# Kernel tuning notes

Hardware: AMD Instinct MI355X
Metric: run time of the kernel (lower is better)

Reference implementation:

```python
import jax, jax.numpy as jnp
import numpy as np

N_NODES = 100000
N_EDGES = 1600000
IN_DIM, FEAT_DIM, HID_DIM, OUT_DIM = 128, 64, 64, 32


def _lin_params(key, fan_in, fan_out, bias=True):
    k1, k2 = jax.random.split(key)
    bound = 1.0 / np.sqrt(fan_in)
    W = jax.random.uniform(k1, (fan_out, fan_in), jnp.float32, -bound, bound)
    if bias:
        b = jax.random.uniform(k2, (fan_out,), jnp.float32, -bound, bound)
        return W, b
    return W


def setup_inputs() -> dict:
    key = jax.random.key(0)
    ks = jax.random.split(key, 10)
    x = jax.random.normal(ks[0], (N_NODES, IN_DIM), jnp.float32)
    edge_index = jax.random.randint(ks[1], (2, N_EDGES), 0, N_NODES, jnp.int64 if jax.config.jax_enable_x64 else jnp.int32)
    W_pre, b_pre = _lin_params(ks[2], IN_DIM, FEAT_DIM)
    Wl1, bl1 = _lin_params(ks[3], FEAT_DIM, HID_DIM)
    Wr1 = _lin_params(ks[4], FEAT_DIM, HID_DIM, bias=False)
    Wl2, bl2 = _lin_params(ks[5], HID_DIM, HID_DIM)
    Wr2 = _lin_params(ks[6], HID_DIM, HID_DIM, bias=False)
    Wl3, bl3 = _lin_params(ks[7], HID_DIM, OUT_DIM)
    Wr3 = _lin_params(ks[8], HID_DIM, OUT_DIM, bias=False)
    return {"x": x, "edge_index": edge_index,
            "W_pre": W_pre, "b_pre": b_pre,
            "Wl1": Wl1, "bl1": bl1, "Wr1": Wr1,
            "Wl2": Wl2, "bl2": bl2, "Wr2": Wr2,
            "Wl3": Wl3, "bl3": bl3, "Wr3": Wr3}


def _sage_conv(x, src, dst, inv_deg, Wl, bl, Wr):
    # mean-aggregate neighbor features per destination node
    summed = jax.ops.segment_sum(x[src], dst, num_segments=N_NODES)  # [N, d]
    agg = summed * inv_deg                                           # [N, d]
    return agg @ Wl.T + bl + x @ Wr.T


def reference(x, edge_index, W_pre, b_pre, Wl1, bl1, Wr1, Wl2, bl2, Wr2, Wl3, bl3, Wr3):
    src, dst = edge_index[0], edge_index[1]
    deg = jax.ops.segment_sum(jnp.ones((N_EDGES,), x.dtype), dst, num_segments=N_NODES)
    inv_deg = (1.0 / jnp.maximum(deg, 1.0))[:, None]  # [N,1]

    h = x @ W_pre.T + b_pre                              # feature_pre
    h = jax.nn.relu(_sage_conv(h, src, dst, inv_deg, Wl1, bl1, Wr1))
    h = jax.nn.relu(_sage_conv(h, src, dst, inv_deg, Wl2, bl2, Wr2))
    h = _sage_conv(h, src, dst, inv_deg, Wl3, bl3, Wr3)
    # F.normalize(p=2, dim=-1)
    norm = jnp.maximum(jnp.linalg.norm(h, axis=-1, keepdims=True), 1e-12)
    return h / norm
```

## Files before the change

### kernel.cpp

```cpp
#include <hip/hip_runtime.h>

#define NN 100000
#define NE 1600000
#define NB 196
#define NPBK 512

static inline size_t alignup(size_t x) { return (x + 255) & ~(size_t)255; }

typedef __attribute__((ext_vector_type(8))) short bfrag;
typedef __attribute__((ext_vector_type(4))) float f32x4v;

__device__ __forceinline__ float bf_lo(unsigned u) { return __uint_as_float(u << 16); }
__device__ __forceinline__ float bf_hi(unsigned u) { return __uint_as_float(u & 0xFFFF0000u); }
__device__ __forceinline__ unsigned short f2bf(float f) {
    unsigned u = __float_as_uint(f);
    return (unsigned short)((u + 0x7FFFu + ((u >> 16) & 1u)) >> 16);
}
__device__ __forceinline__ unsigned pack2(float a, float b) {
    return (unsigned)f2bf(a) | ((unsigned)f2bf(b) << 16);
}

__global__ __launch_bounds__(256) void k_bcount(const int* __restrict__ dst,
                                                int* __restrict__ bcnt) {
    __shared__ int h[NB];
    int tid = threadIdx.x;
    for (int i = tid; i < NB; i += 256) h[i] = 0;
    __syncthreads();
    int i = blockIdx.x * 256 + tid;
    int stride = gridDim.x * 256;
    for (; i < NE; i += stride) atomicAdd(&h[dst[i] >> 9], 1);
    __syncthreads();
    for (int i2 = tid; i2 < NB; i2 += 256) {
        int c = h[i2];
        if (c) atomicAdd(&bcnt[i2], c);
    }
}

__global__ __launch_bounds__(256) void k_bscan(const int* __restrict__ bcnt,
                                               int* __restrict__ bbase,
                                               int* __restrict__ bcur,
                                               int* __restrict__ row_ptr) {
    __shared__ int tmp[256];
    int tid = threadIdx.x;
    int v = (tid < NB) ? bcnt[tid] : 0;
    tmp[tid] = v;
    __syncthreads();
    for (int off = 1; off < 256; off <<= 1) {
        int t = (tid >= off) ? tmp[tid - off] : 0;
        __syncthreads();
        tmp[tid] += t;
        __syncthreads();
    }
    int excl = tmp[tid] - v;
    if (tid < NB) { bbase[tid] = excl; bcur[tid] = excl; }
    if (tid == 0) row_ptr[NN] = NE;
}

#define EPT 16
__global__ __launch_bounds__(256) void k_bscatter(const int* __restrict__ src,
                                                  const int* __restrict__ dst,
                                                  int* __restrict__ bcur,
                                                  unsigned* __restrict__ ebuf) {
    __shared__ int h[NB], base[NB], pos[NB];
    int tid = threadIdx.x;
    for (int i = tid; i < NB; i += 256) h[i] = 0;
    __syncthreads();
    long e0 = (long)blockIdx.x * (256 * EPT);
    unsigned packed[EPT];
    int bk[EPT];
    #pragma unroll
    for (int j = 0; j < EPT; ++j) {
        long e = e0 + (long)j * 256 + tid;
        if (e < NE) {
            int s = src[e], d = dst[e];
            bk[j] = d >> 9;
            packed[j] = ((unsigned)(d & 511) << 17) | (unsigned)s;
            atomicAdd(&h[bk[j]], 1);
        } else bk[j] = -1;
    }
    __syncthreads();
    for (int i = tid; i < NB; i += 256) {
        int c = h[i];
        base[i] = c ? atomicAdd(&bcur[i], c) : 0;
        pos[i] = 0;
    }
    __syncthreads();
    #pragma unroll
    for (int j = 0; j < EPT; ++j) {
        if (bk[j] >= 0) {
            int p = atomicAdd(&pos[bk[j]], 1);
            ebuf[base[bk[j]] + p] = packed[j];
        }
    }
}

__global__ __launch_bounds__(256) void k_bcsr(const unsigned* __restrict__ ebuf,
                                              const int* __restrict__ bbase,
                                              int* __restrict__ row_ptr,
                                              float* __restrict__ inv_deg,
                                              int* __restrict__ col) {
    __shared__ int h[NPBK];
    __shared__ int psum[256];
    int b = blockIdx.x;
    int tid = threadIdx.x;
    int begin = bbase[b];
    int end = (b + 1 < NB) ? bbase[b + 1] : NE;
    for (int i = tid; i < NPBK; i += 256) h[i] = 0;
    __syncthreads();
    for (int e = begin + tid; e < end; e += 256) atomicAdd(&h[ebuf[e] >> 17], 1);
    __syncthreads();
    int a0 = h[2 * tid], a1 = h[2 * tid + 1];
    psum[tid] = a0 + a1;
    __syncthreads();
    for (int off = 1; off < 256; off <<= 1) {
        int t = (tid >= off) ? psum[tid - off] : 0;
        __syncthreads();
        psum[tid] += t;
        __syncthreads();
    }
    int pexcl = psum[tid] - (a0 + a1);
    int eo0 = pexcl, eo1 = pexcl + a0;
    int n0 = b * NPBK + 2 * tid, n1 = n0 + 1;
    if (n0 < NN) { row_ptr[n0] = begin + eo0; inv_deg[n0] = 1.0f / (float)((a0 > 1) ? a0 : 1); }
    if (n1 < NN) { row_ptr[n1] = begin + eo1; inv_deg[n1] = 1.0f / (float)((a1 > 1) ? a1 : 1); }
    __syncthreads();
    h[2 * tid] = eo0;
    h[2 * tid + 1] = eo1;
    __syncthreads();
    for (int e = begin + tid; e < end; e += 256) {
        unsigned p = ebuf[e];
        int dl = p >> 17;
        int s = (int)(p & 0x1FFFFu);
        int q = atomicAdd(&h[dl], 1);
        col[begin + q] = s;
    }
}

template <int K1, int K2, int M, bool RELU, bool NORM, bool ABF, bool OBF>
__global__ __launch_bounds__(256, 2) void k_mfma(const void* __restrict__ A1v,
                                                 const void* __restrict__ A2v,
                                                 const float* __restrict__ W1,
                                                 const float* __restrict__ W2,
                                                 const float* __restrict__ bias,
                                                 void* __restrict__ outv) {
    constexpr int K = K1 + K2;
    static_assert(K == 128, "K must be 128");
    constexpr int NT = M / 16;
    constexpr int SA = 136;
    constexpr int SW = 136;

    __shared__ __align__(16) unsigned short Ahi[64 * SA];
    __shared__ __align__(16) unsigned short Alo[ABF ? 1 : 64 * SA];
    __shared__ __align__(16) unsigned short Whi[M * SW];
    __shared__ __align__(16) unsigned short Wlo[M * SW];

    int tid = threadIdx.x;
    long nbase = (long)blockIdx.x * 64;

    for (int idx = tid; idx < M * 128; idx += 256) {
        int m = idx >> 7, k = idx & 127;
        float w = (K2 == 0 || k < K1) ? W1[m * K1 + k] : W2[m * K2 + (k - K1)];
        unsigned short hb = f2bf(w);
        float hf = __uint_as_float((unsigned)hb << 16);
        Whi[m * SW + k] = hb;
        Wlo[m * SW + k] = f2bf(w - hf);
    }
    if (ABF) {
        const unsigned short* A1 = (const unsigned short*)A1v;
        const unsigned short* A2 = (const unsigned short*)A2v;
        for (int idx = tid; idx < 64 * 16; idx += 256) {
            int row = idx >> 4, c8 = idx & 15;
            long n = nbase + row;
            uint4 v = make_uint4(0u, 0u, 0u, 0u);
            if (n < NN) v = (c8 < 8) ? ((const uint4*)(A1 + n * 64))[c8]
                                     : ((const uint4*)(A2 + n * 64))[c8 - 8];
            *(uint4*)&Ahi[row * SA + c8 * 8] = v;
        }
    } else {
        const float* A1 = (const float*)A1v;
        for (int idx = tid; idx < 64 * 32; idx += 256) {
            int row = idx >> 5, c4 = idx & 31;
            long n = nbase + row;
            float4 v = make_float4(0.f, 0.f, 0.f, 0.f);
            if (n < NN) v = ((const float4*)(A1 + n * 128))[c4];
            ushort4 h, l;
            h.x = f2bf(v.x); l.x = f2bf(v.x - __uint_as_float((unsigned)h.x << 16));
            h.y = f2bf(v.y); l.y = f2bf(v.y - __uint_as_float((unsigned)h.y << 16));
            h.z = f2bf(v.z); l.z = f2bf(v.z - __uint_as_float((unsigned)h.z << 16));
            h.w = f2bf(v.w); l.w = f2bf(v.w - __uint_as_float((unsigned)h.w << 16));
            *(ushort4*)&Ahi[row * SA + c4 * 4] = h;
            *(ushort4*)&Alo[row * SA + c4 * 4] = l;
        }
    }
    __syncthreads();

    const int l = tid & 63, wv = tid >> 6;
    const int row0 = wv * 16;
    const int mrow = l & 15, g = l >> 4;
    const int koff = g * 8;

    bfrag a[4], al[4];
    #pragma unroll
    for (int kk = 0; kk < 4; ++kk)
        a[kk] = *(const bfrag*)&Ahi[(row0 + mrow) * SA + kk * 32 + koff];
    if (!ABF) {
        #pragma unroll
        for (int kk = 0; kk < 4; ++kk)
            al[kk] = *(const bfrag*)&Alo[(row0 + mrow) * SA + kk * 32 + koff];
    }

    f32x4v acc[NT];
    #pragma unroll
    for (int c = 0; c < NT; ++c) {
        float bv = bias[c * 16 + mrow];
        acc[c][0] = bv; acc[c][1] = bv; acc[c][2] = bv; acc[c][3] = bv;
    }

    #pragma unroll
    for (int c = 0; c < NT; ++c) {
        #pragma unroll
        for (int kk = 0; kk < 4; ++kk) {
            bfrag bh = *(const bfrag*)&Whi[(c * 16 + mrow) * SW + kk * 32 + koff];
            bfrag bl = *(const bfrag*)&Wlo[(c * 16 + mrow) * SW + kk * 32 + koff];
            acc[c] = __builtin_amdgcn_mfma_f32_16x16x32_bf16(a[kk], bh, acc[c], 0, 0, 0);
            acc[c] = __builtin_amdgcn_mfma_f32_16x16x32_bf16(a[kk], bl, acc[c], 0, 0, 0);
            if (!ABF)
                acc[c] = __builtin_amdgcn_mfma_f32_16x16x32_bf16(al[kk], bh, acc[c], 0, 0, 0);
        }
    }

    if (RELU) {
        #pragma unroll
        for (int c = 0; c < NT; ++c)
            #pragma unroll
            for (int j = 0; j < 4; ++j) acc[c][j] = fmaxf(acc[c][j], 0.0f);
    }

    if (NORM) {
        #pragma unroll
        for (int j = 0; j < 4; ++j) {
            float s = 0.f;
            #pragma unroll
            for (int c = 0; c < NT; ++c) s += acc[c][j] * acc[c][j];
            s += __shfl_xor(s, 1);
            s += __shfl_xor(s, 2);
            s += __shfl_xor(s, 4);
            s += __shfl_xor(s, 8);
            float sc = 1.0f / fmaxf(sqrtf(s), 1e-12f);
            long n = nbase + row0 + g * 4 + j;
            if (n < NN) {
                float* outf = (float*)outv;
                #pragma unroll
                for (int c = 0; c < NT; ++c)
                    outf[n * M + c * 16 + mrow] = acc[c][j] * sc;
            }
        }
    } else {
        #pragma unroll
        for (int j = 0; j < 4; ++j) {
            long n = nbase + row0 + g * 4 + j;
            if (n >= NN) continue;
            #pragma unroll
            for (int c = 0; c < NT; ++c) {
                if (OBF) ((unsigned short*)outv)[n * M + c * 16 + mrow] = f2bf(acc[c][j]);
                else     ((float*)outv)[n * M + c * 16 + mrow] = acc[c][j];
            }
        }
    }
}

__global__ __launch_bounds__(256) void k_agg16(const unsigned* __restrict__ H,
                                               const int* __restrict__ row_ptr,
                                               const int* __restrict__ col,
                                               const float* __restrict__ inv_deg,
                                               unsigned* __restrict__ AGG) {
    int gt = blockIdx.x * 256 + threadIdx.x;
    int n = gt >> 5;
    int l = gt & 31;
    if (n >= NN) return;
    int beg = row_ptr[n], end = row_ptr[n + 1];
    float a0 = 0.f, a1 = 0.f;
    int e = beg;
    for (; e + 3 < end; e += 4) {
        int s0 = col[e], s1 = col[e + 1], s2 = col[e + 2], s3 = col[e + 3];
        unsigned u0 = H[(long)s0 * 32 + l];
        unsigned u1 = H[(long)s1 * 32 + l];
        unsigned u2 = H[(long)s2 * 32 + l];
        unsigned u3 = H[(long)s3 * 32 + l];
        a0 += bf_lo(u0) + bf_lo(u1) + bf_lo(u2) + bf_lo(u3);
        a1 += bf_hi(u0) + bf_hi(u1) + bf_hi(u2) + bf_hi(u3);
    }
    for (; e < end; ++e) {
        unsigned u = H[(long)col[e] * 32 + l];
        a0 += bf_lo(u);
        a1 += bf_hi(u);
    }
    float w = inv_deg[n];
    AGG[(long)n * 32 + l] = pack2(a0 * w, a1 * w);
}

extern "C" void kernel_launch(void* const* d_in, const int* in_sizes, int n_in,
                              void* d_out, int out_size, void* d_ws, size_t ws_size,
                              hipStream_t stream) {
    const float* x      = (const float*)d_in[0];
    const int*   edges  = (const int*)d_in[1];
    const float* W_pre  = (const float*)d_in[2];
    const float* b_pre  = (const float*)d_in[3];
    const float* Wl1    = (const float*)d_in[4];
    const float* bl1    = (const float*)d_in[5];
    const float* Wr1    = (const float*)d_in[6];
    const float* Wl2    = (const float*)d_in[7];
    const float* bl2    = (const float*)d_in[8];
    const float* Wr2    = (const float*)d_in[9];
    const float* Wl3    = (const float*)d_in[10];
    const float* bl3    = (const float*)d_in[11];
    const float* Wr3    = (const float*)d_in[12];
    float* out = (float*)d_out;

    const int* src = edges;
    const int* dst = edges + NE;

    char* w = (char*)d_ws;
    int*      row_ptr = (int*)w;      w += alignup((NN + 1) * 4);
    float*    inv_deg = (float*)w;    w += alignup(NN * 4);
    int*      bcnt    = (int*)w;      w += alignup(NB * 4);
    int*      bbase   = (int*)w;      w += alignup(NB * 4);
    int*      bcur    = (int*)w;      w += alignup(NB * 4);
    unsigned* ebuf    = (unsigned*)w; w += alignup((size_t)NE * 4);
    int*      col     = (int*)w;      w += alignup((size_t)NE * 4);
    unsigned short* bufA = (unsigned short*)w; w += alignup((size_t)NN * 64 * 2);
    unsigned short* bufB = (unsigned short*)w; w += alignup((size_t)NN * 64 * 2);
    unsigned short* bufC = (unsigned short*)w; w += alignup((size_t)NN * 64 * 2);

    hipMemsetAsync(bcnt, 0, NB * sizeof(int), stream);
    k_bcount<<<1024, 256, 0, stream>>>(dst, bcnt);
    k_bscan<<<1, 256, 0, stream>>>(bcnt, bbase, bcur, row_ptr);
    k_bscatter<<<(NE + 4095) / 4096, 256, 0, stream>>>(src, dst, bcur, ebuf);
    k_bcsr<<<NB, 256, 0, stream>>>(ebuf, bbase, row_ptr, inv_deg, col);

    const int GRID = (NN + 63) / 64;

    k_mfma<128, 0, 64, false, false, false, true>
        <<<GRID, 256, 0, stream>>>(x, nullptr, W_pre, nullptr, b_pre, bufA);

    k_agg16<<<(NN * 32 + 255) / 256, 256, 0, stream>>>((unsigned*)bufA, row_ptr, col, inv_deg, (unsigned*)bufB);
    k_mfma<64, 64, 64, true, false, true, true>
        <<<GRID, 256, 0, stream>>>(bufB, bufA, Wl1, Wr1, bl1, bufC);

    k_agg16<<<(NN * 32 + 255) / 256, 256, 0, stream>>>((unsigned*)bufC, row_ptr, col, inv_deg, (unsigned*)bufB);
    k_mfma<64, 64, 64, true, false, true, true>
        <<<GRID, 256, 0, stream>>>(bufB, bufC, Wl2, Wr2, bl2, bufA);

    k_agg16<<<(NN * 32 + 255) / 256, 256, 0, stream>>>((unsigned*)bufA, row_ptr, col, inv_deg, (unsigned*)bufB);
    k_mfma<64, 64, 32, false, true, true, false>
        <<<GRID, 256, 0, stream>>>(bufB, bufA, Wl3, Wr3, bl3, out);
}
```

Measured before the change: 384.4 us.

## Fuse neighbor mean aggregation into SAGE MFMA kernels

Removes the separate aggregation kernel and the intermediate AGG buffer. Each SAGE-layer block now gathers neighbor rows for its 64 nodes straight into shared memory before the MFMA GEMM, and the gather loop is unrolled by 8. This saves a global write and read of the aggregate plus three launches. In exchange, gather latency now sits inside a GEMM kernel with heavy shared-memory use, so fewer gather threads are in flight (occupancy hint raised to 3 blocks), and degree imbalance within a block can stall the MFMA phase.

```diff
diff --git a/kernel.cpp b/kernel.cpp
--- a/kernel.cpp
+++ b/kernel.cpp
@@ -136,21 +136,13 @@
     }
 }
 
-template <int K1, int K2, int M, bool RELU, bool NORM, bool ABF, bool OBF>
-__global__ __launch_bounds__(256, 2) void k_mfma(const void* __restrict__ A1v,
-                                                 const void* __restrict__ A2v,
-                                                 const float* __restrict__ W1,
-                                                 const float* __restrict__ W2,
-                                                 const float* __restrict__ bias,
-                                                 void* __restrict__ outv) {
-    constexpr int K = K1 + K2;
-    static_assert(K == 128, "K must be 128");
-    constexpr int NT = M / 16;
-    constexpr int SA = 136;
-    constexpr int SW = 136;
-
+__global__ __launch_bounds__(256, 2) void k_pre(const float* __restrict__ X,
+                                                const float* __restrict__ W1,
+                                                const float* __restrict__ bias,
+                                                unsigned short* __restrict__ outb) {
+    constexpr int M = 64, NT = 4, SA = 136, SW = 136;
     __shared__ __align__(16) unsigned short Ahi[64 * SA];
-    __shared__ __align__(16) unsigned short Alo[ABF ? 1 : 64 * SA];
+    __shared__ __align__(16) unsigned short Alo[64 * SA];
     __shared__ __align__(16) unsigned short Whi[M * SW];
     __shared__ __align__(16) unsigned short Wlo[M * SW];
 
@@ -159,38 +151,23 @@
 
     for (int idx = tid; idx < M * 128; idx += 256) {
         int m = idx >> 7, k = idx & 127;
-        float w = (K2 == 0 || k < K1) ? W1[m * K1 + k] : W2[m * K2 + (k - K1)];
+        float w = W1[m * 128 + k];
         unsigned short hb = f2bf(w);
-        float hf = __uint_as_float((unsigned)hb << 16);
         Whi[m * SW + k] = hb;
-        Wlo[m * SW + k] = f2bf(w - hf);
-    }
-    if (ABF) {
-        const unsigned short* A1 = (const unsigned short*)A1v;
-        const unsigned short* A2 = (const unsigned short*)A2v;
-        for (int idx = tid; idx < 64 * 16; idx += 256) {
-            int row = idx >> 4, c8 = idx & 15;
-            long n = nbase + row;
-            uint4 v = make_uint4(0u, 0u, 0u, 0u);
-            if (n < NN) v = (c8 < 8) ? ((const uint4*)(A1 + n * 64))[c8]
-                                     : ((const uint4*)(A2 + n * 64))[c8 - 8];
-            *(uint4*)&Ahi[row * SA + c8 * 8] = v;
-        }
-    } else {
-        const float* A1 = (const float*)A1v;
-        for (int idx = tid; idx < 64 * 32; idx += 256) {
-            int row = idx >> 5, c4 = idx & 31;
-            long n = nbase + row;
-            float4 v = make_float4(0.f, 0.f, 0.f, 0.f);
-            if (n < NN) v = ((const float4*)(A1 + n * 128))[c4];
-            ushort4 h, l;
-            h.x = f2bf(v.x); l.x = f2bf(v.x - __uint_as_float((unsigned)h.x << 16));
-            h.y = f2bf(v.y); l.y = f2bf(v.y - __uint_as_float((unsigned)h.y << 16));
-            h.z = f2bf(v.z); l.z = f2bf(v.z - __uint_as_float((unsigned)h.z << 16));
-            h.w = f2bf(v.w); l.w = f2bf(v.w - __uint_as_float((unsigned)h.w << 16));
-            *(ushort4*)&Ahi[row * SA + c4 * 4] = h;
-            *(ushort4*)&Alo[row * SA + c4 * 4] = l;
-        }
+        Wlo[m * SW + k] = f2bf(w - __uint_as_float((unsigned)hb << 16));
+    }
+    for (int idx = tid; idx < 64 * 32; idx += 256) {
+        int row = idx >> 5, c4 = idx & 31;
+        long n = nbase + row;
+        float4 v = make_float4(0.f, 0.f, 0.f, 0.f);
+        if (n < NN) v = ((const float4*)(X + n * 128))[c4];
+        ushort4 h, l;
+        h.x = f2bf(v.x); l.x = f2bf(v.x - __uint_as_float((unsigned)h.x << 16));
+        h.y = f2bf(v.y); l.y = f2bf(v.y - __uint_as_float((unsigned)h.y << 16));
+        h.z = f2bf(v.z); l.z = f2bf(v.z - __uint_as_float((unsigned)h.z << 16));
+        h.w = f2bf(v.w); l.w = f2bf(v.w - __uint_as_float((unsigned)h.w << 16));
+        *(ushort4*)&Ahi[row * SA + c4 * 4] = h;
+        *(ushort4*)&Alo[row * SA + c4 * 4] = l;
     }
     __syncthreads();
 
@@ -201,12 +178,9 @@
 
     bfrag a[4], al[4];
     #pragma unroll
-    for (int kk = 0; kk < 4; ++kk)
-        a[kk] = *(const bfrag*)&Ahi[(row0 + mrow) * SA + kk * 32 + koff];
-    if (!ABF) {
-        #pragma unroll
-        for (int kk = 0; kk < 4; ++kk)
-            al[kk] = *(const bfrag*)&Alo[(row0 + mrow) * SA + kk * 32 + koff];
+    for (int kk = 0; kk < 4; ++kk) {
+        a[kk]  = *(const bfrag*)&Ahi[(row0 + mrow) * SA + kk * 32 + koff];
+        al[kk] = *(const bfrag*)&Alo[(row0 + mrow) * SA + kk * 32 + koff];
     }
 
     f32x4v acc[NT];
@@ -215,7 +189,6 @@
         float bv = bias[c * 16 + mrow];
         acc[c][0] = bv; acc[c][1] = bv; acc[c][2] = bv; acc[c][3] = bv;
     }
-
     #pragma unroll
     for (int c = 0; c < NT; ++c) {
         #pragma unroll
@@ -224,8 +197,113 @@
             bfrag bl = *(const bfrag*)&Wlo[(c * 16 + mrow) * SW + kk * 32 + koff];
             acc[c] = __builtin_amdgcn_mfma_f32_16x16x32_bf16(a[kk], bh, acc[c], 0, 0, 0);
             acc[c] = __builtin_amdgcn_mfma_f32_16x16x32_bf16(a[kk], bl, acc[c], 0, 0, 0);
-            if (!ABF)
-                acc[c] = __builtin_amdgcn_mfma_f32_16x16x32_bf16(al[kk], bh, acc[c], 0, 0, 0);
+            acc[c] = __builtin_amdgcn_mfma_f32_16x16x32_bf16(al[kk], bh, acc[c], 0, 0, 0);
+        }
+    }
+    #pragma unroll
+    for (int j = 0; j < 4; ++j) {
+        long n = nbase + row0 + g * 4 + j;
+        if (n >= NN) continue;
+        #pragma unroll
+        for (int c = 0; c < NT; ++c)
+            outb[n * 64 + c * 16 + mrow] = f2bf(acc[c][j]);
+    }
+}
+
+template <int M, bool RELU, bool NORM, bool OBF>
+__global__ __launch_bounds__(256, 3) void k_sage(const unsigned short* __restrict__ H,
+                                                 const int* __restrict__ row_ptr,
+                                                 const int* __restrict__ col,
+                                                 const float* __restrict__ inv_deg,
+                                                 const float* __restrict__ Wl,
+                                                 const float* __restrict__ Wr,
+                                                 const float* __restrict__ bias,
+                                                 void* __restrict__ outv) {
+    constexpr int NT = M / 16;
+    constexpr int SA = 136, SW = 136;
+    __shared__ __align__(16) unsigned short Ahi[64 * SA];
+    __shared__ __align__(16) unsigned short Whi[M * SW];
+    __shared__ __align__(16) unsigned short Wlo[M * SW];
+
+    int tid = threadIdx.x;
+    long nbase = (long)blockIdx.x * 64;
+
+    for (int idx = tid; idx < M * 128; idx += 256) {
+        int m = idx >> 7, k = idx & 127;
+        float w = (k < 64) ? Wl[m * 64 + k] : Wr[m * 64 + (k - 64)];
+        unsigned short hb = f2bf(w);
+        Whi[m * SW + k] = hb;
+        Wlo[m * SW + k] = f2bf(w - __uint_as_float((unsigned)hb << 16));
+    }
+    for (int idx = tid; idx < 64 * 8; idx += 256) {
+        int row = idx >> 3, c8 = idx & 7;
+        long n = nbase + row;
+        uint4 v = make_uint4(0u, 0u, 0u, 0u);
+        if (n < NN) v = ((const uint4*)(H + n * 64))[c8];
+        *(uint4*)&Ahi[row * SA + 64 + c8 * 8] = v;
+    }
+    {
+        const unsigned* H32 = (const unsigned*)H;
+        int slot = tid >> 5, l = tid & 31;
+        #pragma unroll
+        for (int it = 0; it < 8; ++it) {
+            int row = it * 8 + slot;
+            long n = nbase + row;
+            float a0 = 0.f, a1 = 0.f;
+            if (n < NN) {
+                int beg = row_ptr[n], end = row_ptr[n + 1];
+                int e = beg;
+                for (; e + 7 < end; e += 8) {
+                    unsigned u0 = H32[(long)col[e + 0] * 32 + l];
+                    unsigned u1 = H32[(long)col[e + 1] * 32 + l];
+                    unsigned u2 = H32[(long)col[e + 2] * 32 + l];
+                    unsigned u3 = H32[(long)col[e + 3] * 32 + l];
+                    unsigned u4 = H32[(long)col[e + 4] * 32 + l];
+                    unsigned u5 = H32[(long)col[e + 5] * 32 + l];
+                    unsigned u6 = H32[(long)col[e + 6] * 32 + l];
+                    unsigned u7 = H32[(long)col[e + 7] * 32 + l];
+                    a0 += bf_lo(u0) + bf_lo(u1) + bf_lo(u2) + bf_lo(u3)
+                        + bf_lo(u4) + bf_lo(u5) + bf_lo(u6) + bf_lo(u7);
+                    a1 += bf_hi(u0) + bf_hi(u1) + bf_hi(u2) + bf_hi(u3)
+                        + bf_hi(u4) + bf_hi(u5) + bf_hi(u6) + bf_hi(u7);
+                }
+                for (; e < end; ++e) {
+                    unsigned u = H32[(long)col[e] * 32 + l];
+                    a0 += bf_lo(u);
+                    a1 += bf_hi(u);
+                }
+                float w = inv_deg[n];
+                a0 *= w; a1 *= w;
+            }
+            *(unsigned*)&Ahi[row * SA + l * 2] = pack2(a0, a1);
+        }
+    }
+    __syncthreads();
+
+    const int l = tid & 63, wv = tid >> 6;
+    const int row0 = wv * 16;
+    const int mrow = l & 15, g = l >> 4;
+    const int koff = g * 8;
+
+    bfrag a[4];
+    #pragma unroll
+    for (int kk = 0; kk < 4; ++kk)
+        a[kk] = *(const bfrag*)&Ahi[(row0 + mrow) * SA + kk * 32 + koff];
+
+    f32x4v acc[NT];
+    #pragma unroll
+    for (int c = 0; c < NT; ++c) {
+        float bv = bias[c * 16 + mrow];
+        acc[c][0] = bv; acc[c][1] = bv; acc[c][2] = bv; acc[c][3] = bv;
+    }
+    #pragma unroll
+    for (int c = 0; c < NT; ++c) {
+        #pragma unroll
+        for (int kk = 0; kk < 4; ++kk) {
+            bfrag bh = *(const bfrag*)&Whi[(c * 16 + mrow) * SW + kk * 32 + koff];
+            bfrag bl = *(const bfrag*)&Wlo[(c * 16 + mrow) * SW + kk * 32 + koff];
+            acc[c] = __builtin_amdgcn_mfma_f32_16x16x32_bf16(a[kk], bh, acc[c], 0, 0, 0);
+            acc[c] = __builtin_amdgcn_mfma_f32_16x16x32_bf16(a[kk], bl, acc[c], 0, 0, 0);
         }
     }
 
@@ -267,36 +345,6 @@
             }
         }
     }
-}
-
-__global__ __launch_bounds__(256) void k_agg16(const unsigned* __restrict__ H,
-                                               const int* __restrict__ row_ptr,
-                                               const int* __restrict__ col,
-                                               const float* __restrict__ inv_deg,
-                                               unsigned* __restrict__ AGG) {
-    int gt = blockIdx.x * 256 + threadIdx.x;
-    int n = gt >> 5;
-    int l = gt & 31;
-    if (n >= NN) return;
-    int beg = row_ptr[n], end = row_ptr[n + 1];
-    float a0 = 0.f, a1 = 0.f;
-    int e = beg;
-    for (; e + 3 < end; e += 4) {
-        int s0 = col[e], s1 = col[e + 1], s2 = col[e + 2], s3 = col[e + 3];
-        unsigned u0 = H[(long)s0 * 32 + l];
-        unsigned u1 = H[(long)s1 * 32 + l];
-        unsigned u2 = H[(long)s2 * 32 + l];
-        unsigned u3 = H[(long)s3 * 32 + l];
-        a0 += bf_lo(u0) + bf_lo(u1) + bf_lo(u2) + bf_lo(u3);
-        a1 += bf_hi(u0) + bf_hi(u1) + bf_hi(u2) + bf_hi(u3);
-    }
-    for (; e < end; ++e) {
-        unsigned u = H[(long)col[e] * 32 + l];
-        a0 += bf_lo(u);
-        a1 += bf_hi(u);
-    }
-    float w = inv_deg[n];
-    AGG[(long)n * 32 + l] = pack2(a0 * w, a1 * w);
 }
 
 extern "C" void kernel_launch(void* const* d_in, const int* in_sizes, int n_in,
@@ -329,7 +377,6 @@
     unsigned* ebuf    = (unsigned*)w; w += alignup((size_t)NE * 4);
     int*      col     = (int*)w;      w += alignup((size_t)NE * 4);
     unsigned short* bufA = (unsigned short*)w; w += alignup((size_t)NN * 64 * 2);
-    unsigned short* bufB = (unsigned short*)w; w += alignup((size_t)NN * 64 * 2);
     unsigned short* bufC = (unsigned short*)w; w += alignup((size_t)NN * 64 * 2);
 
     hipMemsetAsync(bcnt, 0, NB * sizeof(int), stream);
@@ -340,18 +387,14 @@
 
     const int GRID = (NN + 63) / 64;
 
-    k_mfma<128, 0, 64, false, false, false, true>
-        <<<GRID, 256, 0, stream>>>(x, nullptr, W_pre, nullptr, b_pre, bufA);
-
-    k_agg16<<<(NN * 32 + 255) / 256, 256, 0, stream>>>((unsigned*)bufA, row_ptr, col, inv_deg, (unsigned*)bufB);
-    k_mfma<64, 64, 64, true, false, true, true>
-        <<<GRID, 256, 0, stream>>>(bufB, bufA, Wl1, Wr1, bl1, bufC);
-
-    k_agg16<<<(NN * 32 + 255) / 256, 256, 0, stream>>>((unsigned*)bufC, row_ptr, col, inv_deg, (unsigned*)bufB);
-    k_mfma<64, 64, 64, true, false, true, true>
-        <<<GRID, 256, 0, stream>>>(bufB, bufC, Wl2, Wr2, bl2, bufA);
-
-    k_agg16<<<(NN * 32 + 255) / 256, 256, 0, stream>>>((unsigned*)bufA, row_ptr, col, inv_deg, (unsigned*)bufB);
-    k_mfma<64, 64, 32, false, true, true, false>
-        <<<GRID, 256, 0, stream>>>(bufB, bufA, Wl3, Wr3, bl3, out);
-}
+    k_pre<<<GRID, 256, 0, stream>>>(x, W_pre, b_pre, bufA);
+
+    k_sage<64, true, false, true>
+        <<<GRID, 256, 0, stream>>>(bufA, row_ptr, col, inv_deg, Wl1, Wr1, bl1, bufC);
+
+    k_sage<64, true, false, true>
+        <<<GRID, 256, 0, stream>>>(bufC, row_ptr, col, inv_deg, Wl2, Wr2, bl2, bufA);
+
+    k_sage<32, false, true, false>
+        <<<GRID, 256, 0, stream>>>(bufA, row_ptr, col, inv_deg, Wl3, Wr3, bl3, out);
+}
```

Result: slower. 532.3 us (+38.5%).
